# Performance work log

Measured on AMD Instinct MI355X. Metric: run time of the kernel, lower is better.

Reference implementation:

```python
import jax, jax.numpy as jnp
import numpy as np

BETA = 0.25
N_E = 256
E_DIM = 1024


def setup_inputs() -> dict:
    key = jax.random.key(0)
    k1, k2, k3, k4 = jax.random.split(key, 4)
    z = jax.random.normal(k1, (16, E_DIM, 32, 32), dtype=jnp.float32)
    emb = jax.random.normal(k2, (N_E, E_DIM), dtype=jnp.float32)
    conv_w = jax.random.normal(k3, (E_DIM, E_DIM), dtype=jnp.float32) * 0.02
    conv_b = jax.random.normal(k4, (E_DIM,), dtype=jnp.float32) * 0.02
    return {"z": z, "emb": emb, "conv_w": conv_w, "conv_b": conv_b}


def reference(z, emb, conv_w, conv_b):
    # z: [B, C=e_dim, H, W] -> channels-last, flatten spatial+batch
    zp = jnp.transpose(z, (0, 2, 3, 1))          # [B, H, W, C]
    zf = zp.reshape(-1, E_DIM)                    # [N, C]
    # squared L2 distances to codebook: [N, n_e]
    d = (jnp.sum(zf * zf, axis=1, keepdims=True)
         + jnp.sum(emb * emb, axis=1)
         - 2.0 * (zf @ emb.T))
    min_idx = jnp.argmin(d, axis=1)               # [N]
    min_enc = jax.nn.one_hot(min_idx, N_E, dtype=z.dtype)  # [N, n_e]
    z_q = (min_enc @ emb).reshape(zp.shape)       # gather via matmul, as original
    # VQ commitment loss with straight-through estimator
    loss = (jnp.mean((jax.lax.stop_gradient(z_q) - zp) ** 2)
            + BETA * jnp.mean((z_q - jax.lax.stop_gradient(zp)) ** 2))
    z_q = zp + jax.lax.stop_gradient(z_q - zp)
    e_mean = jnp.mean(min_enc, axis=0)
    perplexity = jnp.exp(-jnp.sum(e_mean * jnp.log(e_mean + 1e-10)))
    # back to channels-first, then 1x1 conv (= per-pixel GEMM)
    z_q = jnp.transpose(z_q, (0, 3, 1, 2))        # [B, C, H, W]
    out = jnp.einsum('bchw,oc->bohw', z_q, conv_w) + conv_b[None, :, None, None]
    return out, loss, perplexity, min_idx
```

## Files before the change

### kernel.cpp

```cpp
#include <hip/hip_runtime.h>
#include <math.h>

#define NE 256
#define EDIM 1024
#define HW 1024
#define NPIX 16384
#define OUT_ELEMS 16777216

typedef short short8 __attribute__((ext_vector_type(8)));
typedef float f32x4 __attribute__((ext_vector_type(4)));
typedef float f32x16 __attribute__((ext_vector_type(16)));

#define WS_HIST   0
#define WS_LOSS   1024
#define WS_ZSQ    1028
#define WS_FBITS  2048
#define WS_T      4096
#define WS_MEMSET 1052672
#define WS_CE2    1052672
#define WS_IDX    1053696
#define WS_EH     1119232
#define WS_EL     1643520
#define WS_NEED   2167808

#define DELTA 0.02f

#define WO_CE2  0
#define WO_HIST 1024
#define WO_LOSS 2048
#define WO_IDX  4096
#define WO_T    69632
#define WO_TOTAL 1118208

__device__ __forceinline__ unsigned short f2bf(float f) {
    unsigned u = __float_as_uint(f);
    unsigned r = u + 0x7FFFu + ((u >> 16) & 1u);
    return (unsigned short)(r >> 16);
}
__device__ __forceinline__ float bf2f(unsigned short h) {
    return __uint_as_float(((unsigned)h) << 16);
}

__device__ __forceinline__ void stage16(const void* g, void* l) {
    __builtin_amdgcn_global_load_lds(
        (const __attribute__((address_space(1))) unsigned int*)g,
        (__attribute__((address_space(3))) unsigned int*)l, 16, 0, 0);
}

__global__ __launch_bounds__(64) void k_prep(const float* __restrict__ emb,
                                             unsigned short* __restrict__ eh,
                                             unsigned short* __restrict__ el,
                                             float* __restrict__ ce2) {
    int j = blockIdx.x;
    int l = threadIdx.x;
    const float* row = emb + ((size_t)j << 10);
    float s = 0.f;
    #pragma unroll
    for (int i = 0; i < 4; i++) {
        float4 v = *(const float4*)(row + l * 4 + 256 * i);
        s += v.x * v.x + v.y * v.y + v.z * v.z + v.w * v.w;
        unsigned short h0 = f2bf(v.x), h1 = f2bf(v.y), h2 = f2bf(v.z), h3 = f2bf(v.w);
        uint2 hp, lp;
        hp.x = (unsigned)h0 | ((unsigned)h1 << 16);
        hp.y = (unsigned)h2 | ((unsigned)h3 << 16);
        lp.x = (unsigned)f2bf(v.x - bf2f(h0)) | ((unsigned)f2bf(v.y - bf2f(h1)) << 16);
        lp.y = (unsigned)f2bf(v.z - bf2f(h2)) | ((unsigned)f2bf(v.w - bf2f(h3)) << 16);
        *(uint2*)(eh + ((size_t)j << 10) + l * 4 + 256 * i) = hp;
        *(uint2*)(el + ((size_t)j << 10) + l * 4 + 256 * i) = lp;
    }
    #pragma unroll
    for (int m = 32; m; m >>= 1) s += __shfl_down(s, m, 64);
    if (l == 0) ce2[j] = 0.5f * s;
}

__global__ __launch_bounds__(256) void k_wT(const float* __restrict__ w,
                                            const float* __restrict__ emb,
                                            float* __restrict__ T) {
    __shared__ float wt[64 * 17];
    __shared__ float et[64 * 17];
    int t = threadIdx.x;
    int j0 = blockIdx.x * 64;
    int o0 = blockIdx.y * 64;
    int kb = blockIdx.z * 256;
    int to = t & 15, tj = t >> 4;
    float acc[4][4] = {};
    int lr = t >> 2, lk = (t & 3) * 4;
    for (int kk = kb; kk < kb + 256; kk += 16) {
        float4 wv = *(const float4*)(w + (size_t)(o0 + lr) * EDIM + kk + lk);
        float4 ev = *(const float4*)(emb + (size_t)(j0 + lr) * EDIM + kk + lk);
        __syncthreads();
        wt[lr * 17 + lk + 0] = wv.x; wt[lr * 17 + lk + 1] = wv.y;
        wt[lr * 17 + lk + 2] = wv.z; wt[lr * 17 + lk + 3] = wv.w;
        et[lr * 17 + lk + 0] = ev.x; et[lr * 17 + lk + 1] = ev.y;
        et[lr * 17 + lk + 2] = ev.z; et[lr * 17 + lk + 3] = ev.w;
        __syncthreads();
        #pragma unroll
        for (int k = 0; k < 16; k++) {
            float a[4], b[4];
            #pragma unroll
            for (int i = 0; i < 4; i++) a[i] = wt[(to * 4 + i) * 17 + k];
            #pragma unroll
            for (int i = 0; i < 4; i++) b[i] = et[(tj * 4 + i) * 17 + k];
            #pragma unroll
            for (int i = 0; i < 4; i++)
                #pragma unroll
                for (int jx = 0; jx < 4; jx++) acc[i][jx] += a[i] * b[jx];
        }
    }
    #pragma unroll
    for (int i = 0; i < 4; i++)
        #pragma unroll
        for (int jx = 0; jx < 4; jx++)
            atomicAdd(&T[(size_t)(o0 + to * 4 + i) * NE + j0 + tj * 4 + jx],
                      acc[i][jx]);
}

__global__ __launch_bounds__(256) void k_dist(
        const float* __restrict__ z, const unsigned short* __restrict__ eh,
        const unsigned short* __restrict__ el,
        const float* __restrict__ ce2,
        int* __restrict__ idx_i, float* __restrict__ idx_f,
        int* __restrict__ hist, float* __restrict__ loss_s,
        float* __restrict__ zsq_acc, unsigned int* __restrict__ fbits) {
    __shared__ unsigned short sB3[3][2][256 * 32];
    __shared__ float v1h[2][64], v2h[2][64];
    __shared__ int   i1h[2][64];
    int t = threadIdx.x;
    int lane = t & 63, w = t >> 6;
    int cid = lane & 31, lh = lane >> 5;
    int half = w & 1;
    int pxt = w >> 1;
    int c_base = half << 7;
    int cswz = (cid >> 1) & 3;
    int px0 = blockIdx.x * 64;
    int b = px0 >> 10;
    const float* zp = z + (((size_t)b) << 20) + (px0 & 1023) + pxt * 32 + cid;
    int sc = t >> 2, qp = t & 3;
    int ql = qp ^ ((sc >> 1) & 3);

    f32x16 acc[4];
    #pragma unroll
    for (int nt = 0; nt < 4; nt++)
        #pragma unroll
        for (int i = 0; i < 16; i++) acc[nt][i] = 0.f;

    float zvA[16], zvB[16], zvC[16];
    float zsq = 0.f;

#define STAGE(c, B) do {                                                        \
    int kk_ = (c) * 32;                                                         \
    _Pragma("unroll")                                                           \
    for (int i_ = 0; i_ < 4; i_++) {                                            \
        stage16(eh + (((size_t)(i_ * 64 + sc)) << 10) + kk_ + ql * 8,           \
                &sB3[B][0][(i_ * 256 + w * 64) * 8]);                           \
        stage16(el + (((size_t)(i_ * 64 + sc)) << 10) + kk_ + ql * 8,           \
                &sB3[B][1][(i_ * 256 + w * 64) * 8]);                           \
    } } while (0)

#define ZLOAD(c, ZV) do {                                                       \
    int kk_ = (c) * 32;                                                         \
    _Pragma("unroll")                                                           \
    for (int j_ = 0; j_ < 8; j_++) {                                            \
        ZV[j_]     = zp[((size_t)(kk_ + lh * 8 + j_)) << 10];                   \
        ZV[8 + j_] = zp[((size_t)(kk_ + 16 + lh * 8 + j_)) << 10];              \
    } } while (0)

#define WAITV(n) do {                                                           \
    asm volatile("s_waitcnt vmcnt(" #n ")" ::: "memory");                       \
    __builtin_amdgcn_sched_barrier(0); } while (0)

#define FENCE() do {                                                            \
    asm volatile("" ::: "memory");                                              \
    __builtin_amdgcn_sched_barrier(0); } while (0)

#define BODY(c, B, ZV, PRE, B2, ZV2) do {                                       \
    __builtin_amdgcn_s_barrier();                                               \
    FENCE();                                                                    \
    short8 ah0, al0, ah1, al1;                                                  \
    _Pragma("unroll")                                                           \
    for (int j_ = 0; j_ < 8; j_++) {                                            \
        float z0_ = ZV[j_], z1_ = ZV[8 + j_];                                   \
        zsq += z0_ * z0_ + z1_ * z1_;                                           \
        unsigned short h0_ = f2bf(z0_), h1_ = f2bf(z1_);                        \
        ((unsigned short*)&ah0)[j_] = h0_;                                      \
        ((unsigned short*)&al0)[j_] = f2bf(z0_ - bf2f(h0_));                    \
        ((unsigned short*)&ah1)[j_] = h1_;                                      \
        ((unsigned short*)&al1)[j_] = f2bf(z1_ - bf2f(h1_));                    \
    }                                                                           \
    if (PRE) { STAGE((c) + 2, B2); ZLOAD((c) + 2, ZV2); }                       \
    _Pragma("unroll")                                                           \
    for (int t_ = 0; t_ < 4; t_++) {                                            \
        int crow_ = (c_base + t_ * 32 + cid) * 32;                              \
        int sp0_ = lh ^ cswz;                                                   \
        int sp1_ = (2 + lh) ^ cswz;                                             \
        short8 bh0_ = *(const short8*)&sB3[B][0][crow_ + sp0_ * 8];             \
        short8 bl0_ = *(const short8*)&sB3[B][1][crow_ + sp0_ * 8];             \
        short8 bh1_ = *(const short8*)&sB3[B][0][crow_ + sp1_ * 8];             \
        short8 bl1_ = *(const short8*)&sB3[B][1][crow_ + sp1_ * 8];             \
        acc[t_] = __builtin_amdgcn_mfma_f32_32x32x16_bf16(ah0, bh0_, acc[t_], 0, 0, 0); \
        acc[t_] = __builtin_amdgcn_mfma_f32_32x32x16_bf16(ah0, bl0_, acc[t_], 0, 0, 0); \
        acc[t_] = __builtin_amdgcn_mfma_f32_32x32x16_bf16(al0, bh0_, acc[t_], 0, 0, 0); \
        acc[t_] = __builtin_amdgcn_mfma_f32_32x32x16_bf16(ah1, bh1_, acc[t_], 0, 0, 0); \
        acc[t_] = __builtin_amdgcn_mfma_f32_32x32x16_bf16(ah1, bl1_, acc[t_], 0, 0, 0); \
        acc[t_] = __builtin_amdgcn_mfma_f32_32x32x16_bf16(al1, bh1_, acc[t_], 0, 0, 0); \
    } } while (0)

    STAGE(0, 0); ZLOAD(0, zvA); FENCE();
    STAGE(1, 1); ZLOAD(1, zvB);

    for (int mi = 0; mi < 10; mi++) {
        WAITV(24); BODY(mi * 3 + 0, 0, zvA, 1, 2, zvC);
        WAITV(24); BODY(mi * 3 + 1, 1, zvB, 1, 0, zvA);
        WAITV(24); BODY(mi * 3 + 2, 2, zvC, 1, 1, zvB);
    }
    WAITV(24); BODY(30, 0, zvA, 0, 1, zvB);
    WAITV(0);  BODY(31, 1, zvB, 0, 2, zvC);

#undef STAGE
#undef ZLOAD
#undef WAITV
#undef FENCE
#undef BODY

    #pragma unroll
    for (int msk = 32; msk; msk >>= 1) zsq += __shfl_down(zsq, msk, 64);
    if (half == 0 && lane == 0) atomicAdd(zsq_acc, zsq);

    float c2v[4];
    #pragma unroll
    for (int t_ = 0; t_ < 4; t_++) c2v[t_] = ce2[c_base + t_ * 32 + cid];

    #pragma unroll
    for (int r = 0; r < 16; r++) {
        float v1 = 3.4e38f, v2 = 3.4e38f; int i1 = 0;
        #pragma unroll
        for (int t_ = 0; t_ < 4; t_++) {
            int code = c_base + t_ * 32 + cid;
            float sv = c2v[t_] - acc[t_][r];
            if (sv < v1 || (sv == v1 && code < i1)) { v2 = v1; v1 = sv; i1 = code; }
            else v2 = fminf(v2, sv);
        }
        #pragma unroll
        for (int msk = 1; msk < 32; msk <<= 1) {
            float ov1 = __shfl_xor(v1, msk, 64);
            int   oi1 = __shfl_xor(i1, msk, 64);
            float ov2 = __shfl_xor(v2, msk, 64);
            float nv2 = fminf(fminf(v2, ov2), fmaxf(v1, ov1));
            if (ov1 < v1 || (ov1 == v1 && oi1 < i1)) { v1 = ov1; i1 = oi1; }
            v2 = nv2;
        }
        if (cid == 0) {
            int pl = pxt * 32 + (r & 3) + 8 * (r >> 2) + 4 * lh;
            v1h[half][pl] = v1; v2h[half][pl] = v2; i1h[half][pl] = i1;
        }
    }
    __syncthreads();
    if (half == 1) {
        float lsum = 0.f;
        if (cid == 0) {
            #pragma unroll
            for (int r = 0; r < 16; r++) {
                int pl = pxt * 32 + (r & 3) + 8 * (r >> 2) + 4 * lh;
                float va = v1h[0][pl], v2a = v2h[0][pl];
                int   ia = i1h[0][pl];
                float vb = v1h[1][pl], v2b = v2h[1][pl];
                int   ib = i1h[1][pl];
                float v2m = fminf(fminf(v2a, v2b), fmaxf(va, vb));
                float v1; int i1;
                if (vb < va) { v1 = vb; i1 = ib; }
                else         { v1 = va; i1 = ia; }
                int px = px0 + pl;
                idx_i[px] = i1;
                idx_f[px] = (float)i1;
                atomicAdd(&hist[i1], 1);
                if (v2m - v1 < DELTA)
                    atomicOr(&fbits[px >> 5], 1u << (px & 31));
                lsum += v1;
            }
        }
        lsum += __shfl_xor(lsum, 32, 64);
        if (lane == 0) atomicAdd(loss_s, lsum);
    }
}

__global__ __launch_bounds__(256) void k_cleanup(const float* __restrict__ z,
        const float* __restrict__ emb, const float* __restrict__ ce2,
        const unsigned int* __restrict__ fbits,
        int* __restrict__ idx_i, float* __restrict__ idx_f, int* __restrict__ hist) {
    __shared__ float zs[1024];
    __shared__ float rv[4];
    __shared__ int ri[4];
    int t = threadIdx.x;
    const float* er = emb + (size_t)t * EDIM;
    for (int px = blockIdx.x; px < NPIX; px += gridDim.x) {
        if (!(fbits[px >> 5] & (1u << (px & 31)))) continue;
        int b = px >> 10, p = px & 1023;
        const float* zb = z + (((size_t)b) << 20) + p;
        #pragma unroll
        for (int r = 0; r < 4; r++) {
            int c = t + 256 * r;
            zs[c] = zb[((size_t)c) << 10];
        }
        __syncthreads();
        float d0 = 0.f, d1 = 0.f, d2 = 0.f, d3 = 0.f;
        #pragma unroll 4
        for (int c = 0; c < EDIM; c += 16) {
            float4 e0 = *(const float4*)(er + c);
            float4 e1 = *(const float4*)(er + c + 4);
            float4 e2 = *(const float4*)(er + c + 8);
            float4 e3 = *(const float4*)(er + c + 12);
            d0 += e0.x * zs[c]      + e0.y * zs[c + 1]  + e0.z * zs[c + 2]  + e0.w * zs[c + 3];
            d1 += e1.x * zs[c + 4]  + e1.y * zs[c + 5]  + e1.z * zs[c + 6]  + e1.w * zs[c + 7];
            d2 += e2.x * zs[c + 8]  + e2.y * zs[c + 9]  + e2.z * zs[c + 10] + e2.w * zs[c + 11];
            d3 += e3.x * zs[c + 12] + e3.y * zs[c + 13] + e3.z * zs[c + 14] + e3.w * zs[c + 15];
        }
        float sv = ce2[t] - ((d0 + d1) + (d2 + d3));
        int bi = t;
        #pragma unroll
        for (int msk = 1; msk < 64; msk <<= 1) {
            float ov = __shfl_xor(sv, msk, 64);
            int oi = __shfl_xor(bi, msk, 64);
            if (ov < sv || (ov == sv && oi < bi)) { sv = ov; bi = oi; }
        }
        if ((t & 63) == 0) { rv[t >> 6] = sv; ri[t >> 6] = bi; }
        __syncthreads();
        if (t == 0) {
            float v = rv[0]; int ix = ri[0];
            for (int ww = 1; ww < 4; ww++)
                if (rv[ww] < v || (rv[ww] == v && ri[ww] < ix)) { v = rv[ww]; ix = ri[ww]; }
            int old = idx_i[px];
            if (ix != old) {
                idx_i[px] = ix; idx_f[px] = (float)ix;
                atomicAdd(&hist[ix], 1); atomicSub(&hist[old], 1);
            }
        }
        __syncthreads();
    }
}

__global__ __launch_bounds__(64) void k_norms(const float* __restrict__ emb,
                                              float* __restrict__ ce2) {
    int j = blockIdx.x;
    int lane = threadIdx.x;
    const float* row = emb + (size_t)j * EDIM;
    float s = 0.f;
    #pragma unroll
    for (int i = 0; i < EDIM / 64; i++) {
        float v = row[lane + 64 * i];
        s += v * v;
    }
    #pragma unroll
    for (int m = 32; m; m >>= 1) s += __shfl_down(s, m, 64);
    if (lane == 0) ce2[j] = 0.5f * s;
}

__global__ __launch_bounds__(256) void k_argmin(const float* __restrict__ z,
                                                const float* __restrict__ emb,
                                                const float* __restrict__ ce2,
                                                int* __restrict__ idx_i,
                                                float* __restrict__ idx_f,
                                                int* __restrict__ hist,
                                                float* __restrict__ loss_acc) {
    __shared__ float zt[32 * 64];
    __shared__ float et[256 * 34];
    __shared__ float znorm_s[64];
    int t = threadIdx.x;
    int n0 = blockIdx.x * 64;
    int b = n0 >> 10;
    int p0 = n0 & 1023;
    const float* zb = z + (size_t)b * EDIM * HW;
    int tc = t & 31, tp = t >> 5;
    float acc[8][8] = {};
    float znorm = 0.f;
    for (int kk = 0; kk < EDIM; kk += 32) {
        #pragma unroll
        for (int i = 0; i < 16; i++) {
            int q = t + 256 * i;
            int code = q >> 4, k2 = q & 15;
            float2 v = *(const float2*)(emb + (size_t)code * EDIM + kk + k2 * 2);
            *(float2*)(et + code * 34 + k2 * 2) = v;
        }
        #pragma unroll
        for (int i = 0; i < 4; i++) {
            int q = t + 256 * i;
            int k = q >> 5, p2 = q & 31;
            float2 v = *(const float2*)(zb + (size_t)(kk + k) * HW + p0 + p2 * 2);
            *(float2*)(zt + k * 64 + p2 * 2) = v;
        }
        __syncthreads();
        if (t < 64) {
            #pragma unroll
            for (int k = 0; k < 32; k++) { float zz = zt[k * 64 + t]; znorm += zz * zz; }
        }
        #pragma unroll 4
        for (int k2 = 0; k2 < 16; k2++) {
            float2 ev[8], za[4], zb2[4];
            #pragma unroll
            for (int u = 0; u < 8; u++)
                ev[u] = *(float2*)(et + (tc + 32 * u) * 34 + k2 * 2);
            #pragma unroll
            for (int j = 0; j < 4; j++)
                za[j] = *(float2*)(zt + (2 * k2) * 64 + tp * 8 + 2 * j);
            #pragma unroll
            for (int j = 0; j < 4; j++)
                zb2[j] = *(float2*)(zt + (2 * k2 + 1) * 64 + tp * 8 + 2 * j);
            #pragma unroll
            for (int p = 0; p < 8; p++) {
                float z0 = (p & 1) ? za[p >> 1].y : za[p >> 1].x;
                float z1 = (p & 1) ? zb2[p >> 1].y : zb2[p >> 1].x;
                #pragma unroll
                for (int u = 0; u < 8; u++)
                    acc[p][u] += z0 * ev[u].x + z1 * ev[u].y;
            }
        }
        __syncthreads();
    }
    if (t < 64) znorm_s[t] = znorm;
    float minv[8];
    int mini[8];
    #pragma unroll
    for (int p = 0; p < 8; p++) { minv[p] = 3.4e38f; mini[p] = 0; }
    #pragma unroll
    for (int u = 0; u < 8; u++) {
        int code = tc + 32 * u;
        float cc2 = ce2[code];
        #pragma unroll
        for (int p = 0; p < 8; p++) {
            float s = cc2 - acc[p][u];
            if (s < minv[p] || (s == minv[p] && code < mini[p])) { minv[p] = s; mini[p] = code; }
        }
    }
    #pragma unroll
    for (int m = 1; m < 32; m <<= 1) {
        #pragma unroll
        for (int p = 0; p < 8; p++) {
            float ov = __shfl_xor(minv[p], m, 64);
            int oi = __shfl_xor(mini[p], m, 64);
            if (ov < minv[p] || (ov == minv[p] && oi < mini[p])) { minv[p] = ov; mini[p] = oi; }
        }
    }
    __syncthreads();
    if (tc == 0) {
        float dsum = 0.f;
        #pragma unroll
        for (int p = 0; p < 8; p++) {
            int lp = tp * 8 + p;
            int n = n0 + lp;
            idx_i[n] = mini[p];
            idx_f[n] = (float)mini[p];
            dsum += znorm_s[lp] + 2.f * minv[p];
            atomicAdd(&hist[mini[p]], 1);
        }
        atomicAdd(loss_acc, dsum);
    }
}

__global__ __launch_bounds__(256) void k_scatter(const float* __restrict__ T,
                                                 const float* __restrict__ bias,
                                                 const int* __restrict__ idx,
                                                 float* __restrict__ out) {
    __shared__ float Ts[16 * 256];
    __shared__ float bs[16];
    int t = threadIdx.x;
    int o0 = blockIdx.x * 16;
    int b = blockIdx.y;
    #pragma unroll
    for (int r = 0; r < 16; r++)
        Ts[r * 256 + t] = T[(size_t)(o0 + r) * NE + t];
    if (t < 16) bs[t] = bias[o0 + t];
    __syncthreads();
    int4 i4 = *(const int4*)(idx + b * HW + t * 4);
    #pragma unroll
    for (int r = 0; r < 16; r++) {
        const float* Tr = Ts + r * 256;
        float bb = bs[r];
        float4 v;
        v.x = Tr[i4.x] + bb;
        v.y = Tr[i4.y] + bb;
        v.z = Tr[i4.z] + bb;
        v.w = Tr[i4.w] + bb;
        *(float4*)(out + ((size_t)(b * EDIM + o0 + r) * HW) + t * 4) = v;
    }
}

__global__ __launch_bounds__(256) void k_final_new(const int* __restrict__ hist,
                                                   const float* __restrict__ loss_s,
                                                   const float* __restrict__ zsq,
                                                   float* __restrict__ out) {
    __shared__ float red[4];
    int t = threadIdx.x;
    float em = (float)hist[t] * (1.0f / 16384.0f);
    float v = em * logf(em + 1e-10f);
    #pragma unroll
    for (int m = 32; m; m >>= 1) v += __shfl_down(v, m, 64);
    if ((t & 63) == 0) red[t >> 6] = v;
    __syncthreads();
    if (t == 0) {
        float s = red[0] + red[1] + red[2] + red[3];
        out[OUT_ELEMS] = (zsq[0] + 2.f * loss_s[0]) * 1.25f / 16777216.f;
        out[OUT_ELEMS + 1] = expf(-s);
    }
}

__global__ __launch_bounds__(256) void k_final_old(const int* __restrict__ hist,
                                                   const float* __restrict__ loss_acc,
                                                   float* __restrict__ out) {
    __shared__ float red[4];
    int t = threadIdx.x;
    float em = (float)hist[t] * (1.0f / 16384.0f);
    float v = em * logf(em + 1e-10f);
    #pragma unroll
    for (int m = 32; m; m >>= 1) v += __shfl_down(v, m, 64);
    if ((t & 63) == 0) red[t >> 6] = v;
    __syncthreads();
    if (t == 0) {
        float s = red[0] + red[1] + red[2] + red[3];
        out[OUT_ELEMS] = loss_acc[0] * 1.25f / 16777216.f;
        out[OUT_ELEMS + 1] = expf(-s);
    }
}

extern "C" void kernel_launch(void* const* d_in, const int* in_sizes, int n_in,
                              void* d_out, int out_size, void* d_ws, size_t ws_size,
                              hipStream_t stream) {
    (void)in_sizes; (void)n_in; (void)out_size;
    const float* z      = (const float*)d_in[0];
    const float* emb    = (const float*)d_in[1];
    const float* conv_w = (const float*)d_in[2];
    const float* conv_b = (const float*)d_in[3];
    float* out = (float*)d_out;

    if (ws_size >= WS_NEED) {
        int*   hist     = (int*)((char*)d_ws + WS_HIST);
        float* loss_s   = (float*)((char*)d_ws + WS_LOSS);
        float* zsq      = (float*)((char*)d_ws + WS_ZSQ);
        unsigned int* fbits = (unsigned int*)((char*)d_ws + WS_FBITS);
        float* T        = (float*)((char*)d_ws + WS_T);
        float* ce2      = (float*)((char*)d_ws + WS_CE2);
        int*   idx_i    = (int*)((char*)d_ws + WS_IDX);
        unsigned short* eh = (unsigned short*)((char*)d_ws + WS_EH);
        unsigned short* el = (unsigned short*)((char*)d_ws + WS_EL);
        float* idx_f = out + OUT_ELEMS + 2;

        hipMemsetAsync(d_ws, 0, WS_MEMSET, stream);
        k_prep<<<NE, 64, 0, stream>>>(emb, eh, el, ce2);
        k_wT<<<dim3(4, 16, 4), 256, 0, stream>>>(conv_w, emb, T);
        k_dist<<<256, 256, 0, stream>>>(z, eh, el, ce2, idx_i, idx_f,
                                        hist, loss_s, zsq, fbits);
        k_cleanup<<<256, 256, 0, stream>>>(z, emb, ce2, fbits, idx_i, idx_f, hist);
        k_scatter<<<dim3(64, 16), 256, 0, stream>>>(T, conv_b, idx_i, out);
        k_final_new<<<1, 256, 0, stream>>>(hist, loss_s, zsq, out);
    } else {
        float* ce2      = (float*)((char*)d_ws + WO_CE2);
        int*   hist     = (int*)((char*)d_ws + WO_HIST);
        float* loss_acc = (float*)((char*)d_ws + WO_LOSS);
        int*   idx_i    = (int*)((char*)d_ws + WO_IDX);
        float* T        = (float*)((char*)d_ws + WO_T);
        float* idx_f = out + OUT_ELEMS + 2;

        hipMemsetAsync(d_ws, 0, WO_TOTAL, stream);
        k_norms<<<NE, 64, 0, stream>>>(emb, ce2);
        k_wT<<<dim3(4, 16, 4), 256, 0, stream>>>(conv_w, emb, T);
        k_argmin<<<256, 256, 0, stream>>>(z, emb, ce2, idx_i, idx_f, hist, loss_acc);
        k_scatter<<<dim3(64, 16), 256, 0, stream>>>(T, conv_b, idx_i, out);
        k_final_old<<<1, 256, 0, stream>>>(hist, loss_acc, out);
    }
}
```

Baseline: 260.8 us.

## Split distance kernel into 32-pixel blocks with 4-way code split, double buffering

```diff
diff --git a/kernel.cpp b/kernel.cpp
--- a/kernel.cpp
+++ b/kernel.cpp
@@ -122,29 +122,27 @@
         int* __restrict__ idx_i, float* __restrict__ idx_f,
         int* __restrict__ hist, float* __restrict__ loss_s,
         float* __restrict__ zsq_acc, unsigned int* __restrict__ fbits) {
-    __shared__ unsigned short sB3[3][2][256 * 32];
-    __shared__ float v1h[2][64], v2h[2][64];
-    __shared__ int   i1h[2][64];
+    __shared__ unsigned short sB[2][2][256 * 32];
+    __shared__ float v1h[4][32], v2h[4][32];
+    __shared__ int   i1h[4][32];
     int t = threadIdx.x;
     int lane = t & 63, w = t >> 6;
     int cid = lane & 31, lh = lane >> 5;
-    int half = w & 1;
-    int pxt = w >> 1;
-    int c_base = half << 7;
+    int c_base = w << 6;
     int cswz = (cid >> 1) & 3;
-    int px0 = blockIdx.x * 64;
+    int px0 = blockIdx.x * 32;
     int b = px0 >> 10;
-    const float* zp = z + (((size_t)b) << 20) + (px0 & 1023) + pxt * 32 + cid;
+    const float* zp = z + (((size_t)b) << 20) + (px0 & 1023) + cid;
     int sc = t >> 2, qp = t & 3;
     int ql = qp ^ ((sc >> 1) & 3);
 
-    f32x16 acc[4];
-    #pragma unroll
-    for (int nt = 0; nt < 4; nt++)
+    f32x16 acc[2];
+    #pragma unroll
+    for (int nt = 0; nt < 2; nt++)
         #pragma unroll
         for (int i = 0; i < 16; i++) acc[nt][i] = 0.f;
 
-    float zvA[16], zvB[16], zvC[16];
+    float zvA[16], zvB[16];
     float zsq = 0.f;
 
 #define STAGE(c, B) do {                                                        \
@@ -152,9 +150,9 @@
     _Pragma("unroll")                                                           \
     for (int i_ = 0; i_ < 4; i_++) {                                            \
         stage16(eh + (((size_t)(i_ * 64 + sc)) << 10) + kk_ + ql * 8,           \
-                &sB3[B][0][(i_ * 256 + w * 64) * 8]);                           \
+                &sB[B][0][(i_ * 256 + w * 64) * 8]);                            \
         stage16(el + (((size_t)(i_ * 64 + sc)) << 10) + kk_ + ql * 8,           \
-                &sB3[B][1][(i_ * 256 + w * 64) * 8]);                           \
+                &sB[B][1][(i_ * 256 + w * 64) * 8]);                            \
     } } while (0)
 
 #define ZLOAD(c, ZV) do {                                                       \
@@ -174,6 +172,9 @@
     __builtin_amdgcn_sched_barrier(0); } while (0)
 
 #define BODY(c, B, ZV, PRE, B2, ZV2) do {                                       \
+    WAITV(16);                                                                  \
+    asm volatile("s_waitcnt lgkmcnt(0)" ::: "memory");                          \
+    __builtin_amdgcn_sched_barrier(0);                                          \
     __builtin_amdgcn_s_barrier();                                               \
     FENCE();                                                                    \
     short8 ah0, al0, ah1, al1;                                                  \
@@ -187,16 +188,16 @@
         ((unsigned short*)&ah1)[j_] = h1_;                                      \
         ((unsigned short*)&al1)[j_] = f2bf(z1_ - bf2f(h1_));                    \
     }                                                                           \
-    if (PRE) { STAGE((c) + 2, B2); ZLOAD((c) + 2, ZV2); }                       \
+    if (PRE) { STAGE((c) + 1, B2); FENCE(); ZLOAD((c) + 1, ZV2); }              \
     _Pragma("unroll")                                                           \
-    for (int t_ = 0; t_ < 4; t_++) {                                            \
+    for (int t_ = 0; t_ < 2; t_++) {                                            \
         int crow_ = (c_base + t_ * 32 + cid) * 32;                              \
         int sp0_ = lh ^ cswz;                                                   \
         int sp1_ = (2 + lh) ^ cswz;                                             \
-        short8 bh0_ = *(const short8*)&sB3[B][0][crow_ + sp0_ * 8];             \
-        short8 bl0_ = *(const short8*)&sB3[B][1][crow_ + sp0_ * 8];             \
-        short8 bh1_ = *(const short8*)&sB3[B][0][crow_ + sp1_ * 8];             \
-        short8 bl1_ = *(const short8*)&sB3[B][1][crow_ + sp1_ * 8];             \
+        short8 bh0_ = *(const short8*)&sB[B][0][crow_ + sp0_ * 8];              \
+        short8 bl0_ = *(const short8*)&sB[B][1][crow_ + sp0_ * 8];              \
+        short8 bh1_ = *(const short8*)&sB[B][0][crow_ + sp1_ * 8];              \
+        short8 bl1_ = *(const short8*)&sB[B][1][crow_ + sp1_ * 8];              \
         acc[t_] = __builtin_amdgcn_mfma_f32_32x32x16_bf16(ah0, bh0_, acc[t_], 0, 0, 0); \
         acc[t_] = __builtin_amdgcn_mfma_f32_32x32x16_bf16(ah0, bl0_, acc[t_], 0, 0, 0); \
         acc[t_] = __builtin_amdgcn_mfma_f32_32x32x16_bf16(al0, bh0_, acc[t_], 0, 0, 0); \
@@ -205,16 +206,12 @@
         acc[t_] = __builtin_amdgcn_mfma_f32_32x32x16_bf16(al1, bh1_, acc[t_], 0, 0, 0); \
     } } while (0)
 
-    STAGE(0, 0); ZLOAD(0, zvA); FENCE();
-    STAGE(1, 1); ZLOAD(1, zvB);
-
-    for (int mi = 0; mi < 10; mi++) {
-        WAITV(24); BODY(mi * 3 + 0, 0, zvA, 1, 2, zvC);
-        WAITV(24); BODY(mi * 3 + 1, 1, zvB, 1, 0, zvA);
-        WAITV(24); BODY(mi * 3 + 2, 2, zvC, 1, 1, zvB);
-    }
-    WAITV(24); BODY(30, 0, zvA, 0, 1, zvB);
-    WAITV(0);  BODY(31, 1, zvB, 0, 2, zvC);
+    STAGE(0, 0); FENCE(); ZLOAD(0, zvA);
+
+    for (int mi = 0; mi < 16; mi++) {
+        BODY(2 * mi,     0, zvA, (mi < 15 || 1) && (2 * mi     < 31), 1, zvB);
+        BODY(2 * mi + 1, 1, zvB, (2 * mi + 1 < 31),                   0, zvA);
+    }
 
 #undef STAGE
 #undef ZLOAD
@@ -224,22 +221,19 @@
 
     #pragma unroll
     for (int msk = 32; msk; msk >>= 1) zsq += __shfl_down(zsq, msk, 64);
-    if (half == 0 && lane == 0) atomicAdd(zsq_acc, zsq);
-
-    float c2v[4];
-    #pragma unroll
-    for (int t_ = 0; t_ < 4; t_++) c2v[t_] = ce2[c_base + t_ * 32 + cid];
+    if (w == 0 && lane == 0) atomicAdd(zsq_acc, zsq);
+
+    float c2v[2];
+    #pragma unroll
+    for (int t_ = 0; t_ < 2; t_++) c2v[t_] = ce2[c_base + t_ * 32 + cid];
 
     #pragma unroll
     for (int r = 0; r < 16; r++) {
-        float v1 = 3.4e38f, v2 = 3.4e38f; int i1 = 0;
-        #pragma unroll
-        for (int t_ = 0; t_ < 4; t_++) {
-            int code = c_base + t_ * 32 + cid;
-            float sv = c2v[t_] - acc[t_][r];
-            if (sv < v1 || (sv == v1 && code < i1)) { v2 = v1; v1 = sv; i1 = code; }
-            else v2 = fminf(v2, sv);
-        }
+        float s0 = c2v[0] - acc[0][r];
+        float s1 = c2v[1] - acc[1][r];
+        float v1, v2; int i1;
+        if (s0 <= s1) { v1 = s0; i1 = c_base + cid;      v2 = s1; }
+        else          { v1 = s1; i1 = c_base + 32 + cid; v2 = s0; }
         #pragma unroll
         for (int msk = 1; msk < 32; msk <<= 1) {
             float ov1 = __shfl_xor(v1, msk, 64);
@@ -250,35 +244,35 @@
             v2 = nv2;
         }
         if (cid == 0) {
-            int pl = pxt * 32 + (r & 3) + 8 * (r >> 2) + 4 * lh;
-            v1h[half][pl] = v1; v2h[half][pl] = v2; i1h[half][pl] = i1;
+            int pl = (r & 3) + 8 * (r >> 2) + 4 * lh;
+            v1h[w][pl] = v1; v2h[w][pl] = v2; i1h[w][pl] = i1;
         }
     }
     __syncthreads();
-    if (half == 1) {
+    if (w == 0) {
         float lsum = 0.f;
-        if (cid == 0) {
-            #pragma unroll
-            for (int r = 0; r < 16; r++) {
-                int pl = pxt * 32 + (r & 3) + 8 * (r >> 2) + 4 * lh;
-                float va = v1h[0][pl], v2a = v2h[0][pl];
-                int   ia = i1h[0][pl];
-                float vb = v1h[1][pl], v2b = v2h[1][pl];
-                int   ib = i1h[1][pl];
-                float v2m = fminf(fminf(v2a, v2b), fmaxf(va, vb));
-                float v1; int i1;
-                if (vb < va) { v1 = vb; i1 = ib; }
-                else         { v1 = va; i1 = ia; }
-                int px = px0 + pl;
-                idx_i[px] = i1;
-                idx_f[px] = (float)i1;
-                atomicAdd(&hist[i1], 1);
-                if (v2m - v1 < DELTA)
-                    atomicOr(&fbits[px >> 5], 1u << (px & 31));
-                lsum += v1;
+        if (lane < 32) {
+            int p = lane;
+            float v1 = v1h[0][p], v2 = v2h[0][p];
+            int   i1 = i1h[0][p];
+            #pragma unroll
+            for (int g = 1; g < 4; g++) {
+                float ov1 = v1h[g][p], ov2 = v2h[g][p];
+                int   oi1 = i1h[g][p];
+                float nv2 = fminf(fminf(v2, ov2), fmaxf(v1, ov1));
+                if (ov1 < v1) { v1 = ov1; i1 = oi1; }
+                v2 = nv2;
             }
-        }
-        lsum += __shfl_xor(lsum, 32, 64);
+            int px = px0 + p;
+            idx_i[px] = i1;
+            idx_f[px] = (float)i1;
+            atomicAdd(&hist[i1], 1);
+            if (v2 - v1 < DELTA)
+                atomicOr(&fbits[px >> 5], 1u << (px & 31));
+            lsum = v1;
+        }
+        #pragma unroll
+        for (int msk = 1; msk < 32; msk <<= 1) lsum += __shfl_xor(lsum, msk, 64);
         if (lane == 0) atomicAdd(loss_s, lsum);
     }
 }
@@ -545,7 +539,7 @@
         hipMemsetAsync(d_ws, 0, WS_MEMSET, stream);
         k_prep<<<NE, 64, 0, stream>>>(emb, eh, el, ce2);
         k_wT<<<dim3(4, 16, 4), 256, 0, stream>>>(conv_w, emb, T);
-        k_dist<<<256, 256, 0, stream>>>(z, eh, el, ce2, idx_i, idx_f,
+        k_dist<<<512, 256, 0, stream>>>(z, eh, el, ce2, idx_i, idx_f,
                                         hist, loss_s, zsq, fbits);
         k_cleanup<<<256, 256, 0, stream>>>(z, emb, ce2, fbits, idx_i, idx_f, hist);
         k_scatter<<<dim3(64, 16), 256, 0, stream>>>(T, conv_b, idx_i, out);
```

Result: no change. 262.1 us (+0.5%).
